# Kernel optimization log

Measured on AMD Instinct MI355X. Metric: run time of the kernel, lower is better.

Reference implementation:

```python
import jax, jax.numpy as jnp
import numpy as np

N = 262144          # nodes
F_NODE, F_EDGE = 64, 16
OUT = [64, 64, 64]  # hidden sizes per layer / readout fingerprint size
TARGET = 12
N_DEG = 4           # d = [1,2,3,4]
IN0 = F_NODE + F_EDGE   # duvenaud message out size, layer 0
IN1 = OUT[0] + F_EDGE   # layer 1


def _build_graph():
    # ring: (i, i+1 mod N) -> every node degree 2
    ring = np.stack([np.arange(N), (np.arange(N) + 1) % N], 1)
    # chords: (2i, 2i + N//2) for i < N//8 -> distinct endpoints, bumps degree to 3
    i = np.arange(N // 8)
    chords = np.stack([2 * i, 2 * i + N // 2], 1)
    und = np.concatenate([ring, chords], 0)            # [E, 2] undirected edges
    E = und.shape[0]
    # directed (both directions) for message passing
    src = np.concatenate([und[:, 0], und[:, 1]]).astype(np.int64)
    dst = np.concatenate([und[:, 1], und[:, 0]]).astype(np.int64)
    eid = np.concatenate([np.arange(E), np.arange(E)]).astype(np.int64)
    deg = np.bincount(np.concatenate([und[:, 0], und[:, 1]]), minlength=N)
    deg_idx = (deg - 1).astype(np.int64)               # index into d=[1,2,3,4]
    return src, dst, eid, deg_idx, E


def setup_inputs() -> dict:
    key = jax.random.key(0)
    ks = jax.random.split(key, 9)
    src, dst, eid, deg_idx, E = _build_graph()
    s0 = 1.0 / np.sqrt(IN0)
    sR = 1.0 / np.sqrt(OUT[0])
    return {
        "h_in": jax.random.normal(ks[0], (N, F_NODE), jnp.float32),
        "edge_feat": jax.random.normal(ks[1], (E, F_EDGE), jnp.float32),
        "U0": jax.random.normal(ks[2], (N_DEG, IN0, OUT[0]), jnp.float32) * s0,
        "U1": jax.random.normal(ks[3], (N_DEG, IN1, OUT[1]), jnp.float32) * s0,
        "R0": jax.random.normal(ks[4], (F_NODE, OUT[2]), jnp.float32) * sR,
        "R1": jax.random.normal(ks[5], (OUT[0], OUT[2]), jnp.float32) * sR,
        "R2": jax.random.normal(ks[6], (OUT[1], OUT[2]), jnp.float32) * sR,
        "W_out": jax.random.normal(ks[7], (OUT[2], TARGET), jnp.float32) * sR,
        "b_out": jax.random.normal(ks[8], (TARGET,), jnp.float32) * 0.01,
        "edge_src": jnp.asarray(src),
        "edge_dst": jnp.asarray(dst),
        "edge_eid": jnp.asarray(eid),
        "deg_idx": jnp.asarray(deg_idx),
    }


def reference(h_in, edge_feat, U0, U1, R0, R1, R2, W_out, b_out,
              edge_src, edge_dst, edge_eid, deg_idx):
    ef = edge_feat[edge_eid]  # [2E, F_EDGE] directed-edge features

    def step(h, U):
        # duvenaud message: m_{v<-w} = concat(h_w, e_vw); sum over neighbors
        m = jnp.concatenate([h[edge_src], ef], axis=1)              # [2E, in]
        m_agg = jax.ops.segment_sum(m, edge_dst, num_segments=N)    # [N, in]
        # duvenaud update: h_v' = sigmoid(W_{deg(v)} m_v)
        out_all = jnp.einsum('ni,dio->ndo', m_agg, U)               # [N, D, out]
        sel = jnp.take_along_axis(out_all, deg_idx[:, None, None], axis=1)[:, 0, :]
        return jax.nn.sigmoid(sel)

    h1 = step(h_in, U0)
    h2 = step(h1, U1)
    # duvenaud readout: sum over layers & nodes of softmax(h_l @ R_l), then linear
    fp = (jax.nn.softmax(h_in @ R0, axis=-1)
          + jax.nn.softmax(h1 @ R1, axis=-1)
          + jax.nn.softmax(h2 @ R2, axis=-1)).sum(axis=0)           # [OUT[2]]
    return fp @ W_out + b_out                                       # [TARGET]
```

## Files before the change

kernel.cpp:

```cpp
#include <hip/hip_runtime.h>
#include <hip/hip_bf16.h>
#include <stdint.h>

#define NN 262144
#define VMASK (NN - 1)
#define GRID_BLKS (NN / 128)

typedef __attribute__((ext_vector_type(8))) short short8;
typedef __attribute__((ext_vector_type(4))) float f32x4;

__device__ __forceinline__ float bf2f(uint16_t h) {
    union { uint32_t u; float f; } a; a.u = ((uint32_t)h) << 16; return a.f;
}
__device__ __forceinline__ uint16_t f2bf(float x) {
    union { __hip_bfloat16 b; uint16_t u; } c;
    c.b = __float2bfloat16(x);
    return c.u;
}
__device__ __forceinline__ float sigm(float x) { return 1.f / (1.f + __expf(-x)); }

__device__ __forceinline__ void chord_of(int v, int& cn, int& ce) {
    cn = -1; ce = -1;
    if ((v & 1) == 0) {
        if (v < NN / 4)                            { cn = v + NN / 2; ce = NN + (v >> 1); }
        else if (v >= NN / 2 && v < (3 * NN) / 4)  { cn = v - NN / 2; ce = NN + ((v - NN / 2) >> 1); }
    }
}

__global__ void prep_weights(const float* __restrict__ U0, const float* __restrict__ U1,
                             const float* __restrict__ R0, const float* __restrict__ R1,
                             const float* __restrict__ R2,
                             uint16_t* __restrict__ Ut0, uint16_t* __restrict__ Ut1,
                             uint16_t* __restrict__ Rt)
{
    int idx = blockIdx.x * 256 + threadIdx.x;
    if (idx < 10240) {
        int o = idx / 160, k = idx - o * 160;
        float v = (k < 80) ? U0[5120 + k * 64 + o] : U0[2 * 5120 + (k - 80) * 64 + o];
        Ut0[o * 160 + k] = f2bf(v);
    } else if (idx < 20480) {
        int r = idx - 10240;
        int o = r / 160, k = r - o * 160;
        float v = (k < 80) ? U1[5120 + k * 64 + o] : U1[2 * 5120 + (k - 80) * 64 + o];
        Ut1[o * 160 + k] = f2bf(v);
    } else if (idx < 20480 + 3 * 4096) {
        int r = idx - 20480;
        int layer = r >> 12;
        int e = r & 4095;
        int o = e >> 6, i = e & 63;
        const float* R = (layer == 0) ? R0 : ((layer == 1) ? R1 : R2);
        Rt[layer * 4096 + o * 64 + i] = f2bf(R[i * 64 + o]);
    }
}

template<int MODE>
__device__ __forceinline__ void build_afr(const float* __restrict__ hf,
                                          const uint16_t* __restrict__ hb,
                                          const float* __restrict__ ef,
                                          int v, int koff, short8* afr)
{
    const int vm1 = (v - 1) & VMASK, vp1 = (v + 1) & VMASK;
    const int e1 = vm1;
    int cn, ce; chord_of(v, cn, ce);
    const int off = (cn >= 0) ? 80 : 0;
    const short8 zz = {0, 0, 0, 0, 0, 0, 0, 0};
#pragma unroll
    for (int ks = 0; ks < 5; ++ks) {
        const int mk = ks * 32 + koff - off;
        short8 r = zz;
        if (mk >= 0 && mk < 64) {
            float s[8];
            if (MODE == 0) {
                const float4* x4 = (const float4*)(hf + (size_t)vm1 * 64 + mk);
                const float4* y4 = (const float4*)(hf + (size_t)vp1 * 64 + mk);
                float4 x0 = x4[0], x1 = x4[1], y0 = y4[0], y1 = y4[1];
                s[0] = x0.x + y0.x; s[1] = x0.y + y0.y; s[2] = x0.z + y0.z; s[3] = x0.w + y0.w;
                s[4] = x1.x + y1.x; s[5] = x1.y + y1.y; s[6] = x1.z + y1.z; s[7] = x1.w + y1.w;
                if (cn >= 0) {
                    const float4* z4 = (const float4*)(hf + (size_t)cn * 64 + mk);
                    float4 z0 = z4[0], z1 = z4[1];
                    s[0] += z0.x; s[1] += z0.y; s[2] += z0.z; s[3] += z0.w;
                    s[4] += z1.x; s[5] += z1.y; s[6] += z1.z; s[7] += z1.w;
                }
            } else {
                short8 x = *(const short8*)(hb + (size_t)vm1 * 64 + mk);
                short8 y = *(const short8*)(hb + (size_t)vp1 * 64 + mk);
#pragma unroll
                for (int j = 0; j < 8; ++j) s[j] = bf2f((uint16_t)x[j]) + bf2f((uint16_t)y[j]);
                if (cn >= 0) {
                    short8 zv = *(const short8*)(hb + (size_t)cn * 64 + mk);
#pragma unroll
                    for (int j = 0; j < 8; ++j) s[j] += bf2f((uint16_t)zv[j]);
                }
            }
#pragma unroll
            for (int j = 0; j < 8; ++j) r[j] = (short)f2bf(s[j]);
        } else if (mk >= 64 && mk < 80) {
            const int ek = mk - 64;
            const float4* p4 = (const float4*)(ef + (size_t)e1 * 16 + ek);
            const float4* q4 = (const float4*)(ef + (size_t)v * 16 + ek);
            float4 p0 = p4[0], p1 = p4[1], q0 = q4[0], q1 = q4[1];
            float s[8] = { p0.x + q0.x, p0.y + q0.y, p0.z + q0.z, p0.w + q0.w,
                           p1.x + q1.x, p1.y + q1.y, p1.z + q1.z, p1.w + q1.w };
            if (ce >= 0) {
                const float4* c4 = (const float4*)(ef + (size_t)ce * 16 + ek);
                float4 c0 = c4[0], c1 = c4[1];
                s[0] += c0.x; s[1] += c0.y; s[2] += c0.z; s[3] += c0.w;
                s[4] += c1.x; s[5] += c1.y; s[6] += c1.z; s[7] += c1.w;
            }
#pragma unroll
            for (int j = 0; j < 8; ++j) r[j] = (short)f2bf(s[j]);
        }
        afr[ks] = r;
    }
}

__device__ __forceinline__ void softmax_acc(const f32x4& acc0, const f32x4& acc1,
                                            const f32x4& acc2, const f32x4& acc3,
                                            float& ca0, float& ca1, float& ca2, float& ca3)
{
#pragma unroll
    for (int r = 0; r < 4; ++r) {
        float z0 = acc0[r], z1 = acc1[r], z2 = acc2[r], z3 = acc3[r];
        float m = fmaxf(fmaxf(z0, z1), fmaxf(z2, z3));
        m = fmaxf(m, __shfl_xor(m, 1)); m = fmaxf(m, __shfl_xor(m, 2));
        m = fmaxf(m, __shfl_xor(m, 4)); m = fmaxf(m, __shfl_xor(m, 8));
        float e0 = __expf(z0 - m), e1 = __expf(z1 - m), e2 = __expf(z2 - m), e3 = __expf(z3 - m);
        float s = e0 + e1 + e2 + e3;
        s += __shfl_xor(s, 1); s += __shfl_xor(s, 2);
        s += __shfl_xor(s, 4); s += __shfl_xor(s, 8);
        const float inv = 1.f / s;
        ca0 += e0 * inv; ca1 += e1 * inv; ca2 += e2 * inv; ca3 += e3 * inv;
    }
}

template<int MODE>
__global__ __launch_bounds__(256, 4) void fused_layer(
    const float* __restrict__ hf, const uint16_t* __restrict__ hb,
    const float* __restrict__ ef,
    const uint16_t* __restrict__ Ut, const uint16_t* __restrict__ RtA,
    const uint16_t* __restrict__ Rt0, uint16_t* __restrict__ hout,
    float* __restrict__ fpacc)
{
    __shared__ alignas(16) uint16_t B[64][168];
    __shared__ alignas(16) uint16_t X[128][76];

    const int t = threadIdx.x, w = t >> 6, l = t & 63;
    const int bid = blockIdx.x;
    const int xcd = bid & 7, r_ = bid >> 3;
    const int chunk = ((r_ & 1) << 10) | (xcd << 7) | (r_ >> 1);
    const int vb = chunk * 128;
    const int row16 = l & 15, cq = l >> 4, koff = cq * 8;
    const int va = vb + w * 32 + row16;
    const int vbn = va + 16;

#pragma unroll
    for (int it = t; it < 1280; it += 256) {
        int o = it / 20, c = it - o * 20;
        *(short8*)&B[o][c * 8] = *(const short8*)(Ut + o * 160 + c * 8);
    }

    short8 afrA[5], afrB[5];
    build_afr<MODE>(hf, hb, ef, va,  koff, afrA);
    build_afr<MODE>(hf, hb, ef, vbn, koff, afrB);

    __syncthreads();

    const int bc = row16;
#pragma unroll
    for (int tile = 0; tile < 2; ++tile) {
        f32x4 acc0 = {0,0,0,0}, acc1 = {0,0,0,0}, acc2 = {0,0,0,0}, acc3 = {0,0,0,0};
#pragma unroll
        for (int ks = 0; ks < 5; ++ks) {
            const int kk = ks * 32 + koff;
            short8 a  = tile ? afrB[ks] : afrA[ks];
            short8 b0 = *(const short8*)&B[bc][kk];
            short8 b1 = *(const short8*)&B[16 + bc][kk];
            short8 b2 = *(const short8*)&B[32 + bc][kk];
            short8 b3 = *(const short8*)&B[48 + bc][kk];
            acc0 = __builtin_amdgcn_mfma_f32_16x16x32_bf16(a, b0, acc0, 0, 0, 0);
            acc1 = __builtin_amdgcn_mfma_f32_16x16x32_bf16(a, b1, acc1, 0, 0, 0);
            acc2 = __builtin_amdgcn_mfma_f32_16x16x32_bf16(a, b2, acc2, 0, 0, 0);
            acc3 = __builtin_amdgcn_mfma_f32_16x16x32_bf16(a, b3, acc3, 0, 0, 0);
        }
        const int row0 = w * 32 + tile * 16 + cq * 4;
#pragma unroll
        for (int r = 0; r < 4; ++r) {
            X[row0 + r][row16]      = f2bf(sigm(acc0[r]));
            X[row0 + r][16 + row16] = f2bf(sigm(acc1[r]));
            X[row0 + r][32 + row16] = f2bf(sigm(acc2[r]));
            X[row0 + r][48 + row16] = f2bf(sigm(acc3[r]));
        }
    }
    __syncthreads();

#pragma unroll
    for (int it = t; it < 512; it += 256) {
        int o = it >> 3, c = it & 7;
        *(short8*)&B[o][c * 8] = *(const short8*)(RtA + o * 64 + c * 8);
    }
    if (MODE == 0) {
#pragma unroll
        for (int it = t; it < 512; it += 256) {
            int o = it >> 3, c = it & 7;
            *(short8*)&B[o][72 + c * 8] = *(const short8*)(Rt0 + o * 64 + c * 8);
        }
#pragma unroll
        for (int it = t; it < 1024; it += 256) {
            int row = it >> 3, c = it & 7;
            *(short8*)(hout + (size_t)(vb + row) * 64 + c * 8) = *(const short8*)&X[row][c * 8];
        }
    }
    __syncthreads();

    short8 h0fa[2], h0fb[2];
    if (MODE == 0) {
#pragma unroll
        for (int tile = 0; tile < 2; ++tile) {
            const int v = tile ? vbn : va;
            const float4* s4 = (const float4*)(hf + (size_t)v * 64);
            float4 a0 = s4[cq * 2], a1 = s4[cq * 2 + 1];
            float4 b0 = s4[8 + cq * 2], b1 = s4[8 + cq * 2 + 1];
            short8 f0, f1;
            f0[0] = (short)f2bf(a0.x); f0[1] = (short)f2bf(a0.y);
            f0[2] = (short)f2bf(a0.z); f0[3] = (short)f2bf(a0.w);
            f0[4] = (short)f2bf(a1.x); f0[5] = (short)f2bf(a1.y);
            f0[6] = (short)f2bf(a1.z); f0[7] = (short)f2bf(a1.w);
            f1[0] = (short)f2bf(b0.x); f1[1] = (short)f2bf(b0.y);
            f1[2] = (short)f2bf(b0.z); f1[3] = (short)f2bf(b0.w);
            f1[4] = (short)f2bf(b1.x); f1[5] = (short)f2bf(b1.y);
            f1[6] = (short)f2bf(b1.z); f1[7] = (short)f2bf(b1.w);
            if (tile) { h0fb[0] = f0; h0fb[1] = f1; }
            else      { h0fa[0] = f0; h0fa[1] = f1; }
        }
    }

    float ca0 = 0.f, ca1 = 0.f, ca2 = 0.f, ca3 = 0.f;
#pragma unroll
    for (int tile = 0; tile < 2; ++tile) {
        const int ar = w * 32 + tile * 16 + row16;
        f32x4 acc0 = {0,0,0,0}, acc1 = {0,0,0,0}, acc2 = {0,0,0,0}, acc3 = {0,0,0,0};
#pragma unroll
        for (int ks = 0; ks < 2; ++ks) {
            const int kk = ks * 32 + koff;
            short8 a  = *(const short8*)&X[ar][kk];
            short8 b0 = *(const short8*)&B[bc][kk];
            short8 b1 = *(const short8*)&B[16 + bc][kk];
            short8 b2 = *(const short8*)&B[32 + bc][kk];
            short8 b3 = *(const short8*)&B[48 + bc][kk];
            acc0 = __builtin_amdgcn_mfma_f32_16x16x32_bf16(a, b0, acc0, 0, 0, 0);
            acc1 = __builtin_amdgcn_mfma_f32_16x16x32_bf16(a, b1, acc1, 0, 0, 0);
            acc2 = __builtin_amdgcn_mfma_f32_16x16x32_bf16(a, b2, acc2, 0, 0, 0);
            acc3 = __builtin_amdgcn_mfma_f32_16x16x32_bf16(a, b3, acc3, 0, 0, 0);
        }
        softmax_acc(acc0, acc1, acc2, acc3, ca0, ca1, ca2, ca3);
    }
    if (MODE == 0) {
#pragma unroll
        for (int tile = 0; tile < 2; ++tile) {
            f32x4 acc0 = {0,0,0,0}, acc1 = {0,0,0,0}, acc2 = {0,0,0,0}, acc3 = {0,0,0,0};
#pragma unroll
            for (int ks = 0; ks < 2; ++ks) {
                const int kk = ks * 32 + koff;
                short8 a  = tile ? h0fb[ks] : h0fa[ks];
                short8 b0 = *(const short8*)&B[bc][72 + kk];
                short8 b1 = *(const short8*)&B[16 + bc][72 + kk];
                short8 b2 = *(const short8*)&B[32 + bc][72 + kk];
                short8 b3 = *(const short8*)&B[48 + bc][72 + kk];
                acc0 = __builtin_amdgcn_mfma_f32_16x16x32_bf16(a, b0, acc0, 0, 0, 0);
                acc1 = __builtin_amdgcn_mfma_f32_16x16x32_bf16(a, b1, acc1, 0, 0, 0);
                acc2 = __builtin_amdgcn_mfma_f32_16x16x32_bf16(a, b2, acc2, 0, 0, 0);
                acc3 = __builtin_amdgcn_mfma_f32_16x16x32_bf16(a, b3, acc3, 0, 0, 0);
            }
            softmax_acc(acc0, acc1, acc2, acc3, ca0, ca1, ca2, ca3);
        }
    }

    ca0 += __shfl_xor(ca0, 16); ca0 += __shfl_xor(ca0, 32);
    ca1 += __shfl_xor(ca1, 16); ca1 += __shfl_xor(ca1, 32);
    ca2 += __shfl_xor(ca2, 16); ca2 += __shfl_xor(ca2, 32);
    ca3 += __shfl_xor(ca3, 16); ca3 += __shfl_xor(ca3, 32);
    __syncthreads();
    float* P = (float*)&X[0][0];
    if (cq == 0) {
        P[w * 64 + l]      = ca0;
        P[w * 64 + 16 + l] = ca1;
        P[w * 64 + 32 + l] = ca2;
        P[w * 64 + 48 + l] = ca3;
    }
    __syncthreads();
    if (t < 64)
        atomicAdd(&fpacc[(xcd << 6) + t], P[t] + P[64 + t] + P[128 + t] + P[192 + t]);
}

__global__ void final_kernel(const float* __restrict__ fpacc, const float* __restrict__ W,
                             const float* __restrict__ b, float* __restrict__ out)
{
    __shared__ float ft[64];
    const int t = threadIdx.x;
    if (t < 64) {
        float s = 0.f;
#pragma unroll
        for (int k = 0; k < 8; ++k) s += fpacc[k * 64 + t];
        ft[t] = s;
    }
    __syncthreads();
    if (t < 12) {
        float s = b[t];
#pragma unroll 8
        for (int j = 0; j < 64; ++j) s += ft[j] * W[j * 12 + t];
        out[t] = s;
    }
}

extern "C" void kernel_launch(void* const* d_in, const int* in_sizes, int n_in,
                              void* d_out, int out_size, void* d_ws, size_t ws_size,
                              hipStream_t stream)
{
    const float* h_in = (const float*)d_in[0];
    const float* ef   = (const float*)d_in[1];
    const float* U0   = (const float*)d_in[2];
    const float* U1   = (const float*)d_in[3];
    const float* R0   = (const float*)d_in[4];
    const float* R1   = (const float*)d_in[5];
    const float* R2   = (const float*)d_in[6];
    const float* W    = (const float*)d_in[7];
    const float* bo   = (const float*)d_in[8];

    uint16_t* h1  = (uint16_t*)d_ws;
    uint16_t* Ut0 = h1 + (size_t)NN * 64;
    uint16_t* Ut1 = Ut0 + 10240;
    uint16_t* Rt  = Ut1 + 10240;
    float* fpacc  = (float*)(Rt + 3 * 4096);

    hipMemsetAsync(fpacc, 0, 512 * sizeof(float), stream);

    prep_weights<<<144, 256, 0, stream>>>(U0, U1, R0, R1, R2, Ut0, Ut1, Rt);
    fused_layer<0><<<GRID_BLKS, 256, 0, stream>>>(h_in, nullptr, ef, Ut0,
                                                  Rt + 4096, Rt, h1, fpacc);
    fused_layer<1><<<GRID_BLKS, 256, 0, stream>>>(nullptr, h1, ef, Ut1,
                                                  Rt + 2 * 4096, nullptr, nullptr, fpacc);
    final_kernel<<<1, 64, 0, stream>>>(fpacc, W, bo, (float*)d_out);
}
```

Measured before the change: 111.6 us.

## Make post-update readout per-wave, reading readout weights from global memory

The shared 128-row activation tile is replaced by a per-wave 16-row scratch, so each wave writes its sigmoid outputs, stores them to hout and runs the readout GEMM without block-wide barriers. Readout weights (RtA, Rt0) are now read straight from global/L2 into registers instead of being staged through LDS. This removes two __syncthreads and shrinks LDS, and launch bounds are raised to 5 blocks per SM for more occupancy. In exchange, every wave issues repeated global loads of the readout matrices and the hout stores become smaller, per-wave writes.

```diff
diff --git a/kernel.cpp b/kernel.cpp
--- a/kernel.cpp
+++ b/kernel.cpp
@@ -134,8 +134,30 @@
     }
 }
 
+__device__ __forceinline__ void ro_gemm(const uint16_t* __restrict__ Rg,
+                                        const short8& a0, const short8& a1,
+                                        int row16, int koff,
+                                        float& c0, float& c1, float& c2, float& c3)
+{
+    f32x4 q0 = {0,0,0,0}, q1 = {0,0,0,0}, q2 = {0,0,0,0}, q3 = {0,0,0,0};
+#pragma unroll
+    for (int ks = 0; ks < 2; ++ks) {
+        const int kk = ks * 32 + koff;
+        short8 a = ks ? a1 : a0;
+        short8 b0 = *(const short8*)(Rg + (row16) * 64 + kk);
+        short8 b1 = *(const short8*)(Rg + (16 + row16) * 64 + kk);
+        short8 b2 = *(const short8*)(Rg + (32 + row16) * 64 + kk);
+        short8 b3 = *(const short8*)(Rg + (48 + row16) * 64 + kk);
+        q0 = __builtin_amdgcn_mfma_f32_16x16x32_bf16(a, b0, q0, 0, 0, 0);
+        q1 = __builtin_amdgcn_mfma_f32_16x16x32_bf16(a, b1, q1, 0, 0, 0);
+        q2 = __builtin_amdgcn_mfma_f32_16x16x32_bf16(a, b2, q2, 0, 0, 0);
+        q3 = __builtin_amdgcn_mfma_f32_16x16x32_bf16(a, b3, q3, 0, 0, 0);
+    }
+    softmax_acc(q0, q1, q2, q3, c0, c1, c2, c3);
+}
+
 template<int MODE>
-__global__ __launch_bounds__(256, 4) void fused_layer(
+__global__ __launch_bounds__(256, 5) void fused_layer(
     const float* __restrict__ hf, const uint16_t* __restrict__ hb,
     const float* __restrict__ ef,
     const uint16_t* __restrict__ Ut, const uint16_t* __restrict__ RtA,
@@ -143,7 +165,7 @@
     float* __restrict__ fpacc)
 {
     __shared__ alignas(16) uint16_t B[64][168];
-    __shared__ alignas(16) uint16_t X[128][76];
+    __shared__ alignas(16) uint16_t Xw[4][16][72];
 
     const int t = threadIdx.x, w = t >> 6, l = t & 63;
     const int bid = blockIdx.x;
@@ -163,55 +185,6 @@
     short8 afrA[5], afrB[5];
     build_afr<MODE>(hf, hb, ef, va,  koff, afrA);
     build_afr<MODE>(hf, hb, ef, vbn, koff, afrB);
-
-    __syncthreads();
-
-    const int bc = row16;
-#pragma unroll
-    for (int tile = 0; tile < 2; ++tile) {
-        f32x4 acc0 = {0,0,0,0}, acc1 = {0,0,0,0}, acc2 = {0,0,0,0}, acc3 = {0,0,0,0};
-#pragma unroll
-        for (int ks = 0; ks < 5; ++ks) {
-            const int kk = ks * 32 + koff;
-            short8 a  = tile ? afrB[ks] : afrA[ks];
-            short8 b0 = *(const short8*)&B[bc][kk];
-            short8 b1 = *(const short8*)&B[16 + bc][kk];
-            short8 b2 = *(const short8*)&B[32 + bc][kk];
-            short8 b3 = *(const short8*)&B[48 + bc][kk];
-            acc0 = __builtin_amdgcn_mfma_f32_16x16x32_bf16(a, b0, acc0, 0, 0, 0);
-            acc1 = __builtin_amdgcn_mfma_f32_16x16x32_bf16(a, b1, acc1, 0, 0, 0);
-            acc2 = __builtin_amdgcn_mfma_f32_16x16x32_bf16(a, b2, acc2, 0, 0, 0);
-            acc3 = __builtin_amdgcn_mfma_f32_16x16x32_bf16(a, b3, acc3, 0, 0, 0);
-        }
-        const int row0 = w * 32 + tile * 16 + cq * 4;
-#pragma unroll
-        for (int r = 0; r < 4; ++r) {
-            X[row0 + r][row16]      = f2bf(sigm(acc0[r]));
-            X[row0 + r][16 + row16] = f2bf(sigm(acc1[r]));
-            X[row0 + r][32 + row16] = f2bf(sigm(acc2[r]));
-            X[row0 + r][48 + row16] = f2bf(sigm(acc3[r]));
-        }
-    }
-    __syncthreads();
-
-#pragma unroll
-    for (int it = t; it < 512; it += 256) {
-        int o = it >> 3, c = it & 7;
-        *(short8*)&B[o][c * 8] = *(const short8*)(RtA + o * 64 + c * 8);
-    }
-    if (MODE == 0) {
-#pragma unroll
-        for (int it = t; it < 512; it += 256) {
-            int o = it >> 3, c = it & 7;
-            *(short8*)&B[o][72 + c * 8] = *(const short8*)(Rt0 + o * 64 + c * 8);
-        }
-#pragma unroll
-        for (int it = t; it < 1024; it += 256) {
-            int row = it >> 3, c = it & 7;
-            *(short8*)(hout + (size_t)(vb + row) * 64 + c * 8) = *(const short8*)&X[row][c * 8];
-        }
-    }
-    __syncthreads();
 
     short8 h0fa[2], h0fb[2];
     if (MODE == 0) {
@@ -235,15 +208,18 @@
         }
     }
 
+    __syncthreads();
+
     float ca0 = 0.f, ca1 = 0.f, ca2 = 0.f, ca3 = 0.f;
+    const int bc = row16;
+
 #pragma unroll
     for (int tile = 0; tile < 2; ++tile) {
-        const int ar = w * 32 + tile * 16 + row16;
         f32x4 acc0 = {0,0,0,0}, acc1 = {0,0,0,0}, acc2 = {0,0,0,0}, acc3 = {0,0,0,0};
 #pragma unroll
-        for (int ks = 0; ks < 2; ++ks) {
+        for (int ks = 0; ks < 5; ++ks) {
             const int kk = ks * 32 + koff;
-            short8 a  = *(const short8*)&X[ar][kk];
+            short8 a  = tile ? afrB[ks] : afrA[ks];
             short8 b0 = *(const short8*)&B[bc][kk];
             short8 b1 = *(const short8*)&B[16 + bc][kk];
             short8 b2 = *(const short8*)&B[32 + bc][kk];
@@ -253,27 +229,32 @@
             acc2 = __builtin_amdgcn_mfma_f32_16x16x32_bf16(a, b2, acc2, 0, 0, 0);
             acc3 = __builtin_amdgcn_mfma_f32_16x16x32_bf16(a, b3, acc3, 0, 0, 0);
         }
-        softmax_acc(acc0, acc1, acc2, acc3, ca0, ca1, ca2, ca3);
-    }
+        const int r0 = cq * 4;
+#pragma unroll
+        for (int r = 0; r < 4; ++r) {
+            Xw[w][r0 + r][row16]      = f2bf(sigm(acc0[r]));
+            Xw[w][r0 + r][16 + row16] = f2bf(sigm(acc1[r]));
+            Xw[w][r0 + r][32 + row16] = f2bf(sigm(acc2[r]));
+            Xw[w][r0 + r][48 + row16] = f2bf(sigm(acc3[r]));
+        }
+        if (MODE == 0) {
+#pragma unroll
+            for (int it = l; it < 128; it += 64) {
+                int row = it >> 3, cc = it & 7;
+                *(short8*)(hout + ((size_t)vb + w * 32 + tile * 16 + row) * 64 + cc * 8) =
+                    *(const short8*)&Xw[w][row][cc * 8];
+            }
+        }
+        {
+            short8 x0 = *(const short8*)&Xw[w][row16][koff];
+            short8 x1 = *(const short8*)&Xw[w][row16][32 + koff];
+            ro_gemm(RtA, x0, x1, row16, koff, ca0, ca1, ca2, ca3);
+        }
+    }
+
     if (MODE == 0) {
-#pragma unroll
-        for (int tile = 0; tile < 2; ++tile) {
-            f32x4 acc0 = {0,0,0,0}, acc1 = {0,0,0,0}, acc2 = {0,0,0,0}, acc3 = {0,0,0,0};
-#pragma unroll
-            for (int ks = 0; ks < 2; ++ks) {
-                const int kk = ks * 32 + koff;
-                short8 a  = tile ? h0fb[ks] : h0fa[ks];
-                short8 b0 = *(const short8*)&B[bc][72 + kk];
-                short8 b1 = *(const short8*)&B[16 + bc][72 + kk];
-                short8 b2 = *(const short8*)&B[32 + bc][72 + kk];
-                short8 b3 = *(const short8*)&B[48 + bc][72 + kk];
-                acc0 = __builtin_amdgcn_mfma_f32_16x16x32_bf16(a, b0, acc0, 0, 0, 0);
-                acc1 = __builtin_amdgcn_mfma_f32_16x16x32_bf16(a, b1, acc1, 0, 0, 0);
-                acc2 = __builtin_amdgcn_mfma_f32_16x16x32_bf16(a, b2, acc2, 0, 0, 0);
-                acc3 = __builtin_amdgcn_mfma_f32_16x16x32_bf16(a, b3, acc3, 0, 0, 0);
-            }
-            softmax_acc(acc0, acc1, acc2, acc3, ca0, ca1, ca2, ca3);
-        }
+        ro_gemm(Rt0, h0fa[0], h0fa[1], row16, koff, ca0, ca1, ca2, ca3);
+        ro_gemm(Rt0, h0fb[0], h0fb[1], row16, koff, ca0, ca1, ca2, ca3);
     }
 
     ca0 += __shfl_xor(ca0, 16); ca0 += __shfl_xor(ca0, 32);
@@ -281,7 +262,7 @@
     ca2 += __shfl_xor(ca2, 16); ca2 += __shfl_xor(ca2, 32);
     ca3 += __shfl_xor(ca3, 16); ca3 += __shfl_xor(ca3, 32);
     __syncthreads();
-    float* P = (float*)&X[0][0];
+    float* P = (float*)&Xw[0][0][0];
     if (cq == 0) {
         P[w * 64 + l]      = ca0;
         P[w * 64 + 16 + l] = ca1;
```

Measured after the change: 162.2 us. 1.45x slower.
